# Kernel tuning notes

Hardware: AMD Instinct MI355X
Metric: run time of the kernel (lower is better)

The kernel has to match this reference:

```python
import jax, jax.numpy as jnp
import numpy as np

L, E, K, H, I = 2, 8, 2, 1024, 2048  # stack_size, num_experts, top_k, hidden, intermediate
B, S = 1, 2048


def setup_inputs() -> dict:
    key = jax.random.key(0)
    k0, k1, k2, k3 = jax.random.split(key, 4)
    hidden_states = jax.random.normal(k0, (B, S, H), dtype=jnp.float32)
    router_w = jax.random.normal(k1, (L, H, E), dtype=jnp.float32) * 0.02
    gate_up_proj = jax.random.normal(k2, (L, E, H, 2 * I), dtype=jnp.float32) * (1.0 / np.sqrt(H))
    down_proj = jax.random.normal(k3, (L, E, I, H), dtype=jnp.float32) * (1.0 / np.sqrt(I))
    return {"hidden_states": hidden_states, "router_w": router_w,
            "gate_up_proj": gate_up_proj, "down_proj": down_proj}


def _moe_layer(x, rw, gu_w, dn_w):
    # x: [T,H]; one MoE block: RouterTopK(softmax) + full-capacity top-k GLU expert MLPs
    logits = x @ rw                                   # [T,E] router linear (fp32)
    aff = jax.nn.softmax(logits, axis=-1)
    vals, idx = jax.lax.top_k(aff, K)                 # [T,K]
    vals = vals / jnp.sum(vals, axis=-1, keepdims=True)  # normalize_top_k_affinities=True
    T = x.shape[0]
    # sparse combine weights [T,E]: normalized affinity on chosen experts, 0 elsewhere
    combine = jnp.zeros((T, E), x.dtype).at[jnp.arange(T)[:, None], idx].set(vals)
    gu = jnp.einsum('th,ehi->eti', x, gu_w)           # [E,T,2I] fused gate+up per expert
    gate, up = gu[..., :I], gu[..., I:]
    act = jax.nn.silu(gate) * up                      # GLU with silu
    eo = jnp.einsum('eti,eih->eth', act, dn_w)        # [E,T,H] down proj
    out = jnp.einsum('eth,te->th', eo, combine)       # combine over experts
    return out, logits


def reference(hidden_states, router_w, gate_up_proj, down_proj):
    Bx, Sx, Hx = hidden_states.shape
    x = hidden_states.reshape(-1, Hx)                 # [T,H]
    logits_all = []
    for l in range(L):                                # fixed small stack of layers
        x, logits = _moe_layer(x, router_w[l], gate_up_proj[l], down_proj[l])
        logits_all.append(logits)
    return x.reshape(Bx, Sx, Hx), jnp.stack(logits_all)  # output, [L,T,E] router logits
```

## Files before the change

### kernel.cpp

```cpp
#include <hip/hip_runtime.h>
#include <cstdint>
#include <cstddef>

constexpr int Lc = 2, Ec = 8, Hc = 1024, Ic = 2048, Tc = 2048;

typedef __bf16 bf16x8 __attribute__((ext_vector_type(8)));
typedef float f32x4 __attribute__((ext_vector_type(4)));

__device__ __forceinline__ unsigned short f2bf(float f) {
  unsigned u = __builtin_bit_cast(unsigned, f);
  u = (u + 0x7fffu + ((u >> 16) & 1u)) >> 16;
  return (unsigned short)u;
}
__device__ __forceinline__ float bf2f(unsigned short h) {
  unsigned u = (unsigned)h << 16;
  return __builtin_bit_cast(float, u);
}
__device__ __forceinline__ bf16x8 ldfrag(const unsigned short* p) {
  return __builtin_bit_cast(bf16x8, *(const uint4*)p);
}

__global__ __launch_bounds__(256) void router_kernel(
    const float* __restrict__ x, const float* __restrict__ rw, float* __restrict__ logits,
    unsigned short* __restrict__ xh, unsigned short* __restrict__ xl) {
  const int t = blockIdx.x;
  const int tid = threadIdx.x;
  const float* xr = x + (size_t)t * Hc;
  const int h0 = tid * 4;
  const float4 v = *(const float4*)(xr + h0);
  const float f[4] = {v.x, v.y, v.z, v.w};
  unsigned short hs[4], ls[4];
#pragma unroll
  for (int j = 0; j < 4; ++j) {
    hs[j] = f2bf(f[j]);
    ls[j] = f2bf(f[j] - bf2f(hs[j]));
  }
  *(uint2*)(xh + (size_t)t * Hc + h0) =
      uint2{(unsigned)hs[0] | ((unsigned)hs[1] << 16), (unsigned)hs[2] | ((unsigned)hs[3] << 16)};
  *(uint2*)(xl + (size_t)t * Hc + h0) =
      uint2{(unsigned)ls[0] | ((unsigned)ls[1] << 16), (unsigned)ls[2] | ((unsigned)ls[3] << 16)};

  float acc[Ec];
#pragma unroll
  for (int e = 0; e < Ec; ++e) acc[e] = 0.f;
#pragma unroll
  for (int j = 0; j < 4; ++j) {
    const float* w = rw + (size_t)(h0 + j) * Ec;
#pragma unroll
    for (int e = 0; e < Ec; ++e) acc[e] += f[j] * w[e];
  }
  __shared__ float red[256][Ec];
#pragma unroll
  for (int e = 0; e < Ec; ++e) red[tid][e] = acc[e];
  __syncthreads();
  for (int s = 128; s > 0; s >>= 1) {
    if (tid < s) {
#pragma unroll
      for (int e = 0; e < Ec; ++e) red[tid][e] += red[tid + s][e];
    }
    __syncthreads();
  }
  if (tid < Ec) logits[(size_t)t * Ec + tid] = red[0][tid];
}

__global__ void topk_kernel(const float* __restrict__ logits, int* __restrict__ cnt,
                            int* __restrict__ tokList, float* __restrict__ wList) {
  const int t = blockIdx.x * blockDim.x + threadIdx.x;
  if (t >= Tc) return;
  float l[Ec];
#pragma unroll
  for (int e = 0; e < Ec; ++e) l[e] = logits[(size_t)t * Ec + e];
  float b0 = -3.4e38f, b1 = -3.4e38f;
  int i0 = 0, i1 = 0;
#pragma unroll
  for (int e = 0; e < Ec; ++e) {
    if (l[e] > b0) { b1 = b0; i1 = i0; b0 = l[e]; i0 = e; }
    else if (l[e] > b1) { b1 = l[e]; i1 = e; }
  }
  const float w0 = 1.f / (1.f + expf(b1 - b0));
  const float w1 = 1.f - w0;
  int p0 = atomicAdd(&cnt[i0], 1);
  tokList[i0 * Tc + p0] = t;
  wList[i0 * Tc + p0] = w0;
  int p1 = atomicAdd(&cnt[i1], 1);
  tokList[i1 * Tc + p1] = t;
  wList[i1 * Tc + p1] = w1;
}

__global__ void offsets_kernel(const int* __restrict__ cnt, int* __restrict__ off) {
  if (threadIdx.x == 0) {
    int s = 0;
    for (int e = 0; e < Ec; ++e) { off[e] = s; s += cnt[e]; }
  }
}

template <bool SPLIT>
__global__ __launch_bounds__(256) void wconv_kernel(const float* __restrict__ src,
                                                    unsigned short* __restrict__ dh,
                                                    unsigned short* __restrict__ dl,
                                                    int K, int N) {
  const int e = blockIdx.z;
  const int n0 = blockIdx.x * 64;
  const int k0 = blockIdx.y * 64;
  const int NB = N >> 6, KS = K >> 5;
  src += (size_t)e * K * N;

  __shared__ unsigned short lh[64][66];
  __shared__ unsigned short ll[SPLIT ? 64 : 1][66];
  const int tid = threadIdx.x;

  {
    const int r = tid >> 2, cg = (tid & 3) * 16;
    const float* sp = src + (size_t)(k0 + r) * N + n0 + cg;
#pragma unroll
    for (int i = 0; i < 16; i += 4) {
      const float4 v = *(const float4*)(sp + i);
      const float f[4] = {v.x, v.y, v.z, v.w};
#pragma unroll
      for (int j = 0; j < 4; ++j) {
        const unsigned short h = f2bf(f[j]);
        lh[r][cg + i + j] = h;
        if constexpr (SPLIT) ll[r][cg + i + j] = f2bf(f[j] - bf2f(h));
      }
    }
  }
  __syncthreads();
  {
    const int ksl = tid >> 7, q = (tid >> 5) & 3, n2 = (tid & 31) * 2;
    const int kb = ksl * 32 + q * 8;
    union { unsigned short s[16]; uint4 u[2]; } oh, ol;
#pragma unroll
    for (int s = 0; s < 2; ++s)
#pragma unroll
      for (int i = 0; i < 8; ++i) {
        oh.s[s * 8 + i] = lh[kb + i][n2 + s];
        if constexpr (SPLIT) ol.s[s * 8 + i] = ll[kb + i][n2 + s];
      }
    const size_t cb =
        (((size_t)e * NB + (n0 >> 6)) * KS + (k0 >> 5) + ksl) * 2048 + q * 512 + n2 * 8;
    *(uint4*)(dh + cb) = oh.u[0];
    *(uint4*)(dh + cb + 8) = oh.u[1];
    if constexpr (SPLIT) {
      *(uint4*)(dl + cb) = ol.u[0];
      *(uint4*)(dl + cb + 8) = ol.u[1];
    }
  }
}

template <bool SPLIT>
__global__ __launch_bounds__(256, SPLIT ? 3 : 4) void gateup_kernel(
    const unsigned short* __restrict__ xh, const unsigned short* __restrict__ xl,
    const unsigned short* __restrict__ gwSh, const unsigned short* __restrict__ gwSl,
    const int* __restrict__ cnt, const int* __restrict__ off,
    const int* __restrict__ tokList, unsigned short* __restrict__ actH,
    unsigned short* __restrict__ actL) {
  const int d = blockIdx.x;
  const int lid = (d & 7) * ((int)gridDim.x >> 3) + (d >> 3);
  const int mi = lid & 15;
  const int e = (lid >> 4) & 7;
  const int nb = lid >> 7;
  const int M = cnt[e];
  const int m0 = mi * 128;
  if (m0 >= M) return;
  const int tid = threadIdx.x;
  const int wv = tid >> 6, l64 = tid & 63;
  const int q = l64 >> 4, mr = l64 & 15;
  const int nc = wv * 16 + mr;

  __shared__ __align__(16) unsigned short sAh[2][128 * 40];
  __shared__ __align__(16) unsigned short sAl[2][SPLIT ? 128 * 40 : 8];

  const size_t fragoff = (size_t)(q * 64 + nc) * 8;
  const size_t gBase = (((size_t)e * 64 + nb) * 32) * 2048 + fragoff;
  const size_t uBase = (((size_t)e * 64 + nb + 32) * 32) * 2048 + fragoff;

  const int ar = tid >> 2, ak = (tid & 3) * 8;
  int r0 = m0 + ar;      if (r0 >= M) r0 = M - 1;
  int r1 = m0 + 64 + ar; if (r1 >= M) r1 = M - 1;
  const size_t a0o = (size_t)tokList[e * Tc + r0] * Hc + ak;
  const size_t a1o = (size_t)tokList[e * Tc + r1] * Hc + ak;

  f32x4 accg[8], accu[8];
#pragma unroll
  for (int i = 0; i < 8; ++i) {
    accg[i] = f32x4{0.f, 0.f, 0.f, 0.f};
    accu[i] = f32x4{0.f, 0.f, 0.f, 0.f};
  }

  uint4 paA0h{}, paA1h{}, paA0l{}, paA1l{};
  uint4 paB0h{}, paB1h{}, paB0l{}, paB1l{};
  bf16x8 bcAgh{}, bcAuh{}, bcAgl{}, bcAul{};
  bf16x8 bcBgh{}, bcBuh{}, bcBgl{}, bcBul{};

  paA0h = *(const uint4*)(xh + a0o);
  paA1h = *(const uint4*)(xh + a1o);
  if constexpr (SPLIT) {
    paA0l = *(const uint4*)(xl + a0o);
    paA1l = *(const uint4*)(xl + a1o);
  }
  *(uint4*)&sAh[0][ar * 40 + ak] = paA0h;
  *(uint4*)&sAh[0][(ar + 64) * 40 + ak] = paA1h;
  if constexpr (SPLIT) {
    *(uint4*)&sAl[0][ar * 40 + ak] = paA0l;
    *(uint4*)&sAl[0][(ar + 64) * 40 + ak] = paA1l;
  }
  bcAgh = ldfrag(gwSh + gBase);
  bcAuh = ldfrag(gwSh + uBase);
  if constexpr (SPLIT) {
    bcAgl = ldfrag(gwSl + gBase);
    bcAul = ldfrag(gwSl + uBase);
  }
  paA0h = *(const uint4*)(xh + a0o + 32);
  paA1h = *(const uint4*)(xh + a1o + 32);
  if constexpr (SPLIT) {
    paA0l = *(const uint4*)(xl + a0o + 32);
    paA1l = *(const uint4*)(xl + a1o + 32);
  }
  asm volatile("s_waitcnt lgkmcnt(0)" ::: "memory");
  __builtin_amdgcn_s_barrier();

#define GU_STEP(T, CUR, NX, PA0H, PA1H, PA0L, PA1L, PN0H, PN1H, PN0L, PN1L,             \
                BCGH, BCUH, BCGL, BCUL, BNGH, BNUH, BNGL, BNUL)                         \
  {                                                                                     \
    if ((T) + 1 < 32) {                                                                 \
      BNGH = ldfrag(gwSh + gBase + (size_t)((T) + 1) * 2048);                           \
      BNUH = ldfrag(gwSh + uBase + (size_t)((T) + 1) * 2048);                           \
      if constexpr (SPLIT) {                                                            \
        BNGL = ldfrag(gwSl + gBase + (size_t)((T) + 1) * 2048);                         \
        BNUL = ldfrag(gwSl + uBase + (size_t)((T) + 1) * 2048);                         \
      }                                                                                 \
    }                                                                                   \
    if ((T) + 2 < 32) {                                                                 \
      PN0H = *(const uint4*)(xh + a0o + ((T) + 2) * 32);                                \
      PN1H = *(const uint4*)(xh + a1o + ((T) + 2) * 32);                                \
      if constexpr (SPLIT) {                                                            \
        PN0L = *(const uint4*)(xl + a0o + ((T) + 2) * 32);                              \
        PN1L = *(const uint4*)(xl + a1o + ((T) + 2) * 32);                              \
      }                                                                                 \
    }                                                                                   \
    if ((T) + 1 < 32) {                                                                 \
      *(uint4*)&sAh[NX][ar * 40 + ak] = PA0H;                                           \
      *(uint4*)&sAh[NX][(ar + 64) * 40 + ak] = PA1H;                                    \
      if constexpr (SPLIT) {                                                            \
        *(uint4*)&sAl[NX][ar * 40 + ak] = PA0L;                                         \
        *(uint4*)&sAl[NX][(ar + 64) * 40 + ak] = PA1L;                                  \
      }                                                                                 \
    }                                                                                   \
    __builtin_amdgcn_s_setprio(1);                                                      \
    _Pragma("unroll")                                                                   \
    for (int mt = 0; mt < 8; ++mt) {                                                    \
      const bf16x8 ah = ldfrag(&sAh[CUR][(mt * 16 + mr) * 40 + q * 8]);                 \
      accg[mt] = __builtin_amdgcn_mfma_f32_16x16x32_bf16(ah, BCGH, accg[mt], 0, 0, 0);  \
      accu[mt] = __builtin_amdgcn_mfma_f32_16x16x32_bf16(ah, BCUH, accu[mt], 0, 0, 0);  \
      if constexpr (SPLIT) {                                                            \
        const bf16x8 alr = ldfrag(&sAl[CUR][(mt * 16 + mr) * 40 + q * 8]);              \
        accg[mt] = __builtin_amdgcn_mfma_f32_16x16x32_bf16(ah, BCGL, accg[mt], 0, 0, 0);\
        accg[mt] = __builtin_amdgcn_mfma_f32_16x16x32_bf16(alr, BCGH, accg[mt], 0, 0, 0);\
        accu[mt] = __builtin_amdgcn_mfma_f32_16x16x32_bf16(ah, BCUL, accu[mt], 0, 0, 0);\
        accu[mt] = __builtin_amdgcn_mfma_f32_16x16x32_bf16(alr, BCUH, accu[mt], 0, 0, 0);\
      }                                                                                 \
    }                                                                                   \
    __builtin_amdgcn_s_setprio(0);                                                      \
    if ((T) < 31) {                                                                     \
      asm volatile("s_waitcnt lgkmcnt(0)" ::: "memory");                                \
      __builtin_amdgcn_s_barrier();                                                     \
    }                                                                                   \
  }

  for (int t = 0; t < 32; t += 2) {
    GU_STEP(t, 0, 1, paA0h, paA1h, paA0l, paA1l, paB0h, paB1h, paB0l, paB1l,
            bcAgh, bcAuh, bcAgl, bcAul, bcBgh, bcBuh, bcBgl, bcBul)
    GU_STEP(t + 1, 1, 0, paB0h, paB1h, paB0l, paB1l, paA0h, paA1h, paA0l, paA1l,
            bcBgh, bcBuh, bcBgl, bcBul, bcAgh, bcAuh, bcAgl, bcAul)
  }
#undef GU_STEP

  const int valid = M - m0;
  const int rowbase = off[e] + m0;
#pragma unroll
  for (int mt = 0; mt < 8; ++mt) {
#pragma unroll
    for (int r = 0; r < 4; ++r) {
      const int row = mt * 16 + q * 4 + r;
      if (row < valid) {
        const float g = accg[mt][r];
        const float u = accu[mt][r];
        const float a = (g / (1.f + expf(-g))) * u;
        const size_t idx = (size_t)(rowbase + row) * Ic + (nb * 64 + nc);
        const unsigned short h = f2bf(a);
        actH[idx] = h;
        if constexpr (SPLIT) actL[idx] = f2bf(a - bf2f(h));
      }
    }
  }
}

template <bool SPLIT>
__global__ __launch_bounds__(256, 4) void down_kernel(
    const unsigned short* __restrict__ actH, const unsigned short* __restrict__ actL,
    const unsigned short* __restrict__ dwSh, const unsigned short* __restrict__ dwSl,
    const int* __restrict__ cnt, const int* __restrict__ off,
    const int* __restrict__ tokList, const float* __restrict__ wList,
    float* __restrict__ out) {
  const int d = blockIdx.x;
  const int lid = (d & 7) * ((int)gridDim.x >> 3) + (d >> 3);
  const int mi = lid & 15;
  const int e = (lid >> 4) & 7;
  const int nb = lid >> 7;
  const int M = cnt[e];
  const int m0 = mi * 128;
  if (m0 >= M) return;
  const int tid = threadIdx.x;
  const int wv = tid >> 6, l64 = tid & 63;
  const int q = l64 >> 4, mr = l64 & 15;
  const int nc = wv * 16 + mr;

  __shared__ __align__(16) unsigned short sAh[2][128 * 40];
  __shared__ __align__(16) unsigned short sAl[2][SPLIT ? 128 * 40 : 8];
  __shared__ int sTok[128];
  __shared__ float sW[128];

  if (tid < 128) {
    int r = m0 + tid;
    int rc = r < M ? r : M - 1;
    sTok[tid] = tokList[e * Tc + rc];
    sW[tid] = wList[e * Tc + rc];
  }

  const size_t fragoff = (size_t)(q * 64 + nc) * 8;
  const size_t bBase = (((size_t)e * 16 + nb) * 64) * 2048 + fragoff;
  const int offE = off[e];

  const int ar = tid >> 2, ak = (tid & 3) * 8;
  int r0 = m0 + ar;      if (r0 >= M) r0 = M - 1;
  int r1 = m0 + 64 + ar; if (r1 >= M) r1 = M - 1;
  const size_t a0o = (size_t)(offE + r0) * Ic + ak;
  const size_t a1o = (size_t)(offE + r1) * Ic + ak;

  f32x4 acc[8];
#pragma unroll
  for (int i = 0; i < 8; ++i) acc[i] = f32x4{0.f, 0.f, 0.f, 0.f};

  uint4 paA0h{}, paA1h{}, paA0l{}, paA1l{};
  uint4 paB0h{}, paB1h{}, paB0l{}, paB1l{};
  bf16x8 bcAh{}, bcAl{}, bcBh{}, bcBl{};

  paA0h = *(const uint4*)(actH + a0o);
  paA1h = *(const uint4*)(actH + a1o);
  if constexpr (SPLIT) {
    paA0l = *(const uint4*)(actL + a0o);
    paA1l = *(const uint4*)(actL + a1o);
  }
  *(uint4*)&sAh[0][ar * 40 + ak] = paA0h;
  *(uint4*)&sAh[0][(ar + 64) * 40 + ak] = paA1h;
  if constexpr (SPLIT) {
    *(uint4*)&sAl[0][ar * 40 + ak] = paA0l;
    *(uint4*)&sAl[0][(ar + 64) * 40 + ak] = paA1l;
  }
  bcAh = ldfrag(dwSh + bBase);
  if constexpr (SPLIT) bcAl = ldfrag(dwSl + bBase);
  paA0h = *(const uint4*)(actH + a0o + 32);
  paA1h = *(const uint4*)(actH + a1o + 32);
  if constexpr (SPLIT) {
    paA0l = *(const uint4*)(actL + a0o + 32);
    paA1l = *(const uint4*)(actL + a1o + 32);
  }
  asm volatile("s_waitcnt lgkmcnt(0)" ::: "memory");
  __builtin_amdgcn_s_barrier();

#define DN_STEP(T, CUR, NX, PA0H, PA1H, PA0L, PA1L, PN0H, PN1H, PN0L, PN1L,             \
                BCH, BCL, BNH, BNL)                                                     \
  {                                                                                     \
    if ((T) + 1 < 64) {                                                                 \
      BNH = ldfrag(dwSh + bBase + (size_t)((T) + 1) * 2048);                            \
      if constexpr (SPLIT) BNL = ldfrag(dwSl + bBase + (size_t)((T) + 1) * 2048);       \
    }                                                                                   \
    if ((T) + 2 < 64) {                                                                 \
      PN0H = *(const uint4*)(actH + a0o + ((T) + 2) * 32);                              \
      PN1H = *(const uint4*)(actH + a1o + ((T) + 2) * 32);                              \
      if constexpr (SPLIT) {                                                            \
        PN0L = *(const uint4*)(actL + a0o + ((T) + 2) * 32);                            \
        PN1L = *(const uint4*)(actL + a1o + ((T) + 2) * 32);                            \
      }                                                                                 \
    }                                                                                   \
    if ((T) + 1 < 64) {                                                                 \
      *(uint4*)&sAh[NX][ar * 40 + ak] = PA0H;                                           \
      *(uint4*)&sAh[NX][(ar + 64) * 40 + ak] = PA1H;                                    \
      if constexpr (SPLIT) {                                                            \
        *(uint4*)&sAl[NX][ar * 40 + ak] = PA0L;                                         \
        *(uint4*)&sAl[NX][(ar + 64) * 40 + ak] = PA1L;                                  \
      }                                                                                 \
    }                                                                                   \
    __builtin_amdgcn_s_setprio(1);                                                      \
    _Pragma("unroll")                                                                   \
    for (int mt = 0; mt < 8; ++mt) {                                                    \
      const bf16x8 ah = ldfrag(&sAh[CUR][(mt * 16 + mr) * 40 + q * 8]);                 \
      acc[mt] = __builtin_amdgcn_mfma_f32_16x16x32_bf16(ah, BCH, acc[mt], 0, 0, 0);     \
      if constexpr (SPLIT) {                                                            \
        const bf16x8 alr = ldfrag(&sAl[CUR][(mt * 16 + mr) * 40 + q * 8]);              \
        acc[mt] = __builtin_amdgcn_mfma_f32_16x16x32_bf16(ah, BCL, acc[mt], 0, 0, 0);   \
        acc[mt] = __builtin_amdgcn_mfma_f32_16x16x32_bf16(alr, BCH, acc[mt], 0, 0, 0);  \
      }                                                                                 \
    }                                                                                   \
    __builtin_amdgcn_s_setprio(0);                                                      \
    if ((T) < 63) {                                                                     \
      asm volatile("s_waitcnt lgkmcnt(0)" ::: "memory");                                \
      __builtin_amdgcn_s_barrier();                                                     \
    }                                                                                   \
  }

  for (int t = 0; t < 64; t += 2) {
    DN_STEP(t, 0, 1, paA0h, paA1h, paA0l, paA1l, paB0h, paB1h, paB0l, paB1l,
            bcAh, bcAl, bcBh, bcBl)
    DN_STEP(t + 1, 1, 0, paB0h, paB1h, paB0l, paB1l, paA0h, paA1h, paA0l, paA1l,
            bcBh, bcBl, bcAh, bcAl)
  }
#undef DN_STEP

  const int valid = M - m0;
#pragma unroll
  for (int mt = 0; mt < 8; ++mt) {
#pragma unroll
    for (int r = 0; r < 4; ++r) {
      const int row = mt * 16 + q * 4 + r;
      if (row < valid) {
        atomicAdd(&out[(size_t)sTok[row] * Hc + (nb * 64 + nc)], sW[row] * acc[mt][r]);
      }
    }
  }
}

extern "C" void kernel_launch(void* const* d_in, const int* in_sizes, int n_in, void* d_out,
                              int out_size, void* d_ws, size_t ws_size, hipStream_t stream) {
  const float* x_in = (const float*)d_in[0];
  const float* rw = (const float*)d_in[1];
  const float* guw = (const float*)d_in[2];
  const float* dnw = (const float*)d_in[3];
  float* out = (float*)d_out;
  float* logits_base = out + (size_t)Tc * Hc;

  uint8_t* w = (uint8_t*)d_ws;
  float* x1 = (float*)w;                    w += (size_t)Tc * Hc * 4;
  unsigned short* xh = (unsigned short*)w;  w += (size_t)Tc * Hc * 2;
  unsigned short* xl = (unsigned short*)w;  w += (size_t)Tc * Hc * 2;
  unsigned short* actH = (unsigned short*)w; w += (size_t)Tc * 2 * Ic * 2;
  unsigned short* actL = (unsigned short*)w; w += (size_t)Tc * 2 * Ic * 2;
  int* tokList = (int*)w;                   w += (size_t)Ec * Tc * 4;
  float* wList = (float*)w;                 w += (size_t)Ec * Tc * 4;
  int* cnt0 = (int*)w;                      w += 64;
  int* cnt1 = (int*)w;                      w += 64;
  int* off = (int*)w;                       w += 64;
  unsigned short* wTh = (unsigned short*)w; w += (size_t)Ec * 2 * Ic * Hc * 2;
  unsigned short* wTl = (unsigned short*)w; w += (size_t)Ec * 2 * Ic * Hc * 2;

  hipMemsetAsync(cnt0, 0, 192, stream);
  hipMemsetAsync(x1, 0, (size_t)Tc * Hc * 4, stream);
  hipMemsetAsync(out, 0, (size_t)Tc * Hc * 4, stream);

  router_kernel<<<Tc, 256, 0, stream>>>(x_in, rw, logits_base, xh, xl);
  topk_kernel<<<Tc / 256, 256, 0, stream>>>(logits_base, cnt0, tokList, wList);
  offsets_kernel<<<1, 64, 0, stream>>>(cnt0, off);
  wconv_kernel<true><<<dim3(2 * Ic / 64, Hc / 64, Ec), 256, 0, stream>>>(guw, wTh, wTl, Hc, 2 * Ic);
  gateup_kernel<true><<<16 * 32 * Ec, 256, 0, stream>>>(xh, xl, wTh, wTl, cnt0, off,
                                                        tokList, actH, actL);
  wconv_kernel<true><<<dim3(Hc / 64, Ic / 64, Ec), 256, 0, stream>>>(dnw, wTh, wTl, Ic, Hc);
  down_kernel<true><<<16 * 16 * Ec, 256, 0, stream>>>(actH, actL, wTh, wTl, cnt0,
                                                      off, tokList, wList, x1);

  const float* rw1 = rw + (size_t)Hc * Ec;
  const float* guw1 = guw + (size_t)Ec * Hc * 2 * Ic;
  const float* dnw1 = dnw + (size_t)Ec * Ic * Hc;
  router_kernel<<<Tc, 256, 0, stream>>>(x1, rw1, logits_base + (size_t)Tc * Ec, xh, xl);
  topk_kernel<<<Tc / 256, 256, 0, stream>>>(logits_base + (size_t)Tc * Ec, cnt1, tokList, wList);
  offsets_kernel<<<1, 64, 0, stream>>>(cnt1, off);
  wconv_kernel<false><<<dim3(2 * Ic / 64, Hc / 64, Ec), 256, 0, stream>>>(guw1, wTh, wTl, Hc, 2 * Ic);
  gateup_kernel<false><<<16 * 32 * Ec, 256, 0, stream>>>(xh, xl, wTh, wTl, cnt1, off,
                                                         tokList, actH, actL);
  wconv_kernel<false><<<dim3(Hc / 64, Ic / 64, Ec), 256, 0, stream>>>(dnw1, wTh, wTl, Ic, Hc);
  down_kernel<false><<<16 * 16 * Ec, 256, 0, stream>>>(actH, actL, wTh, wTl, cnt1,
                                                       off, tokList, wList, out);
}
```

Before: 935.2 us.

## Fuse weight conversion blocks into router, gate-up and down kernels

Removes the standalone weight-conversion launches. Each upcoming weight conversion now runs as extra blocks appended to the grid of the preceding compute kernel, so conversion overlaps the router, gate-up or down GEMM and fills idle compute units. Separate A and B weight buffers are used so conversion for the next stage does not overwrite weights still being read. The cost is larger grids, a shared-memory union that may change occupancy, and competition for memory bandwidth with the GEMM blocks.

```diff
diff --git a/kernel.cpp b/kernel.cpp
--- a/kernel.cpp
+++ b/kernel.cpp
@@ -20,10 +20,79 @@
   return __builtin_bit_cast(bf16x8, *(const uint4*)p);
 }
 
+template <bool WSPLIT>
+__device__ __forceinline__ void wconv_block(const float* __restrict__ src,
+                                            unsigned short* __restrict__ dh,
+                                            unsigned short* __restrict__ dl,
+                                            int K, int N, int idx, char* smem) {
+  const int nN = N >> 6, nK = K >> 6;
+  const int sN = 31 - __builtin_clz((unsigned)nN);
+  const int sK = 31 - __builtin_clz((unsigned)nK);
+  const int bx = idx & (nN - 1);
+  const int by = (idx >> sN) & (nK - 1);
+  const int e = idx >> (sN + sK);
+  const int n0 = bx * 64, k0 = by * 64;
+  const int NB = N >> 6, KS = K >> 5;
+  src += (size_t)e * K * N;
+
+  unsigned short(*lh)[66] = (unsigned short(*)[66])smem;
+  unsigned short(*ll)[66] = (unsigned short(*)[66])(smem + 64 * 66 * 2);
+  const int tid = threadIdx.x;
+
+  {
+    const int r = tid >> 2, cg = (tid & 3) * 16;
+    const float* sp = src + (size_t)(k0 + r) * N + n0 + cg;
+#pragma unroll
+    for (int i = 0; i < 16; i += 4) {
+      const float4 v = *(const float4*)(sp + i);
+      const float f[4] = {v.x, v.y, v.z, v.w};
+#pragma unroll
+      for (int j = 0; j < 4; ++j) {
+        const unsigned short h = f2bf(f[j]);
+        lh[r][cg + i + j] = h;
+        if constexpr (WSPLIT) ll[r][cg + i + j] = f2bf(f[j] - bf2f(h));
+      }
+    }
+  }
+  __syncthreads();
+  {
+    const int ksl = tid >> 7, q = (tid >> 5) & 3, n2 = (tid & 31) * 2;
+    const int kb = ksl * 32 + q * 8;
+    union { unsigned short s[16]; uint4 u[2]; } oh, ol;
+#pragma unroll
+    for (int s = 0; s < 2; ++s)
+#pragma unroll
+      for (int i = 0; i < 8; ++i) {
+        oh.s[s * 8 + i] = lh[kb + i][n2 + s];
+        if constexpr (WSPLIT) ol.s[s * 8 + i] = ll[kb + i][n2 + s];
+      }
+    const size_t cb =
+        (((size_t)e * NB + (n0 >> 6)) * KS + (k0 >> 5) + ksl) * 2048 + q * 512 + n2 * 8;
+    *(uint4*)(dh + cb) = oh.u[0];
+    *(uint4*)(dh + cb + 8) = oh.u[1];
+    if constexpr (WSPLIT) {
+      *(uint4*)(dl + cb) = ol.u[0];
+      *(uint4*)(dl + cb + 8) = ol.u[1];
+    }
+  }
+}
+
+template <bool WFUSE>
 __global__ __launch_bounds__(256) void router_kernel(
     const float* __restrict__ x, const float* __restrict__ rw, float* __restrict__ logits,
-    unsigned short* __restrict__ xh, unsigned short* __restrict__ xl) {
-  const int t = blockIdx.x;
+    unsigned short* __restrict__ xh, unsigned short* __restrict__ xl,
+    const float* __restrict__ wsrc, unsigned short* __restrict__ wdh,
+    unsigned short* __restrict__ wdl, int WK, int WN) {
+  __shared__ __align__(16) char smem[WFUSE ? 16896 : 8192];
+  const int bid = blockIdx.x;
+  if constexpr (WFUSE) {
+    if (bid >= Tc) {
+      wconv_block<true>(wsrc, wdh, wdl, WK, WN, bid - Tc, smem);
+      return;
+    }
+  }
+  float(*red)[Ec] = (float(*)[Ec])smem;
+  const int t = bid;
   const int tid = threadIdx.x;
   const float* xr = x + (size_t)t * Hc;
   const int h0 = tid * 4;
@@ -49,7 +118,6 @@
 #pragma unroll
     for (int e = 0; e < Ec; ++e) acc[e] += f[j] * w[e];
   }
-  __shared__ float red[256][Ec];
 #pragma unroll
   for (int e = 0; e < Ec; ++e) red[tid][e] = acc[e];
   __syncthreads();
@@ -94,68 +162,24 @@
   }
 }
 
-template <bool SPLIT>
-__global__ __launch_bounds__(256) void wconv_kernel(const float* __restrict__ src,
-                                                    unsigned short* __restrict__ dh,
-                                                    unsigned short* __restrict__ dl,
-                                                    int K, int N) {
-  const int e = blockIdx.z;
-  const int n0 = blockIdx.x * 64;
-  const int k0 = blockIdx.y * 64;
-  const int NB = N >> 6, KS = K >> 5;
-  src += (size_t)e * K * N;
-
-  __shared__ unsigned short lh[64][66];
-  __shared__ unsigned short ll[SPLIT ? 64 : 1][66];
-  const int tid = threadIdx.x;
-
-  {
-    const int r = tid >> 2, cg = (tid & 3) * 16;
-    const float* sp = src + (size_t)(k0 + r) * N + n0 + cg;
-#pragma unroll
-    for (int i = 0; i < 16; i += 4) {
-      const float4 v = *(const float4*)(sp + i);
-      const float f[4] = {v.x, v.y, v.z, v.w};
-#pragma unroll
-      for (int j = 0; j < 4; ++j) {
-        const unsigned short h = f2bf(f[j]);
-        lh[r][cg + i + j] = h;
-        if constexpr (SPLIT) ll[r][cg + i + j] = f2bf(f[j] - bf2f(h));
-      }
-    }
-  }
-  __syncthreads();
-  {
-    const int ksl = tid >> 7, q = (tid >> 5) & 3, n2 = (tid & 31) * 2;
-    const int kb = ksl * 32 + q * 8;
-    union { unsigned short s[16]; uint4 u[2]; } oh, ol;
-#pragma unroll
-    for (int s = 0; s < 2; ++s)
-#pragma unroll
-      for (int i = 0; i < 8; ++i) {
-        oh.s[s * 8 + i] = lh[kb + i][n2 + s];
-        if constexpr (SPLIT) ol.s[s * 8 + i] = ll[kb + i][n2 + s];
-      }
-    const size_t cb =
-        (((size_t)e * NB + (n0 >> 6)) * KS + (k0 >> 5) + ksl) * 2048 + q * 512 + n2 * 8;
-    *(uint4*)(dh + cb) = oh.u[0];
-    *(uint4*)(dh + cb + 8) = oh.u[1];
-    if constexpr (SPLIT) {
-      *(uint4*)(dl + cb) = ol.u[0];
-      *(uint4*)(dl + cb + 8) = ol.u[1];
-    }
-  }
-}
-
-template <bool SPLIT>
+template <bool SPLIT, bool WFUSE, bool WSPLIT>
 __global__ __launch_bounds__(256, SPLIT ? 3 : 4) void gateup_kernel(
     const unsigned short* __restrict__ xh, const unsigned short* __restrict__ xl,
     const unsigned short* __restrict__ gwSh, const unsigned short* __restrict__ gwSl,
     const int* __restrict__ cnt, const int* __restrict__ off,
     const int* __restrict__ tokList, unsigned short* __restrict__ actH,
-    unsigned short* __restrict__ actL) {
+    unsigned short* __restrict__ actL, const float* __restrict__ wsrc,
+    unsigned short* __restrict__ wdh, unsigned short* __restrict__ wdl, int WK, int WN) {
+  constexpr int GB = 4096;
+  __shared__ __align__(16) char smem[SPLIT ? 40960 : 20480];
   const int d = blockIdx.x;
-  const int lid = (d & 7) * ((int)gridDim.x >> 3) + (d >> 3);
+  if constexpr (WFUSE) {
+    if (d >= GB) {
+      wconv_block<WSPLIT>(wsrc, wdh, wdl, WK, WN, d - GB, smem);
+      return;
+    }
+  }
+  const int lid = (d & 7) * (GB >> 3) + (d >> 3);
   const int mi = lid & 15;
   const int e = (lid >> 4) & 7;
   const int nb = lid >> 7;
@@ -167,8 +191,8 @@
   const int q = l64 >> 4, mr = l64 & 15;
   const int nc = wv * 16 + mr;
 
-  __shared__ __align__(16) unsigned short sAh[2][128 * 40];
-  __shared__ __align__(16) unsigned short sAl[2][SPLIT ? 128 * 40 : 8];
+  unsigned short* sAh = (unsigned short*)smem;
+  unsigned short* sAl = (unsigned short*)(SPLIT ? smem + 20480 : smem);
 
   const size_t fragoff = (size_t)(q * 64 + nc) * 8;
   const size_t gBase = (((size_t)e * 64 + nb) * 32) * 2048 + fragoff;
@@ -198,11 +222,11 @@
     paA0l = *(const uint4*)(xl + a0o);
     paA1l = *(const uint4*)(xl + a1o);
   }
-  *(uint4*)&sAh[0][ar * 40 + ak] = paA0h;
-  *(uint4*)&sAh[0][(ar + 64) * 40 + ak] = paA1h;
-  if constexpr (SPLIT) {
-    *(uint4*)&sAl[0][ar * 40 + ak] = paA0l;
-    *(uint4*)&sAl[0][(ar + 64) * 40 + ak] = paA1l;
+  *(uint4*)&sAh[ar * 40 + ak] = paA0h;
+  *(uint4*)&sAh[(ar + 64) * 40 + ak] = paA1h;
+  if constexpr (SPLIT) {
+    *(uint4*)&sAl[ar * 40 + ak] = paA0l;
+    *(uint4*)&sAl[(ar + 64) * 40 + ak] = paA1l;
   }
   bcAgh = ldfrag(gwSh + gBase);
   bcAuh = ldfrag(gwSh + uBase);
@@ -239,21 +263,21 @@
       }                                                                                 \
     }                                                                                   \
     if ((T) + 1 < 32) {                                                                 \
-      *(uint4*)&sAh[NX][ar * 40 + ak] = PA0H;                                           \
-      *(uint4*)&sAh[NX][(ar + 64) * 40 + ak] = PA1H;                                    \
-      if constexpr (SPLIT) {                                                            \
-        *(uint4*)&sAl[NX][ar * 40 + ak] = PA0L;                                         \
-        *(uint4*)&sAl[NX][(ar + 64) * 40 + ak] = PA1L;                                  \
+      *(uint4*)&sAh[(NX) * 5120 + ar * 40 + ak] = PA0H;                                 \
+      *(uint4*)&sAh[(NX) * 5120 + (ar + 64) * 40 + ak] = PA1H;                          \
+      if constexpr (SPLIT) {                                                            \
+        *(uint4*)&sAl[(NX) * 5120 + ar * 40 + ak] = PA0L;                               \
+        *(uint4*)&sAl[(NX) * 5120 + (ar + 64) * 40 + ak] = PA1L;                        \
       }                                                                                 \
     }                                                                                   \
     __builtin_amdgcn_s_setprio(1);                                                      \
     _Pragma("unroll")                                                                   \
     for (int mt = 0; mt < 8; ++mt) {                                                    \
-      const bf16x8 ah = ldfrag(&sAh[CUR][(mt * 16 + mr) * 40 + q * 8]);                 \
+      const bf16x8 ah = ldfrag(&sAh[(CUR) * 5120 + (mt * 16 + mr) * 40 + q * 8]);       \
       accg[mt] = __builtin_amdgcn_mfma_f32_16x16x32_bf16(ah, BCGH, accg[mt], 0, 0, 0);  \
       accu[mt] = __builtin_amdgcn_mfma_f32_16x16x32_bf16(ah, BCUH, accu[mt], 0, 0, 0);  \
       if constexpr (SPLIT) {                                                            \
-        const bf16x8 alr = ldfrag(&sAl[CUR][(mt * 16 + mr) * 40 + q * 8]);              \
+        const bf16x8 alr = ldfrag(&sAl[(CUR) * 5120 + (mt * 16 + mr) * 40 + q * 8]);    \
         accg[mt] = __builtin_amdgcn_mfma_f32_16x16x32_bf16(ah, BCGL, accg[mt], 0, 0, 0);\
         accg[mt] = __builtin_amdgcn_mfma_f32_16x16x32_bf16(alr, BCGH, accg[mt], 0, 0, 0);\
         accu[mt] = __builtin_amdgcn_mfma_f32_16x16x32_bf16(ah, BCUL, accu[mt], 0, 0, 0);\
@@ -295,15 +319,26 @@
   }
 }
 
-template <bool SPLIT>
+template <bool SPLIT, bool WFUSE, bool WSPLIT>
 __global__ __launch_bounds__(256, 4) void down_kernel(
     const unsigned short* __restrict__ actH, const unsigned short* __restrict__ actL,
     const unsigned short* __restrict__ dwSh, const unsigned short* __restrict__ dwSl,
     const int* __restrict__ cnt, const int* __restrict__ off,
     const int* __restrict__ tokList, const float* __restrict__ wList,
-    float* __restrict__ out) {
+    float* __restrict__ out, const float* __restrict__ wsrc,
+    unsigned short* __restrict__ wdh, unsigned short* __restrict__ wdl, int WK, int WN) {
+  constexpr int GB = 2048;
+  __shared__ __align__(16) char smem[SPLIT ? 40960 : 20480];
+  __shared__ int sTok[128];
+  __shared__ float sW[128];
   const int d = blockIdx.x;
-  const int lid = (d & 7) * ((int)gridDim.x >> 3) + (d >> 3);
+  if constexpr (WFUSE) {
+    if (d >= GB) {
+      wconv_block<WSPLIT>(wsrc, wdh, wdl, WK, WN, d - GB, smem);
+      return;
+    }
+  }
+  const int lid = (d & 7) * (GB >> 3) + (d >> 3);
   const int mi = lid & 15;
   const int e = (lid >> 4) & 7;
   const int nb = lid >> 7;
@@ -315,10 +350,8 @@
   const int q = l64 >> 4, mr = l64 & 15;
   const int nc = wv * 16 + mr;
 
-  __shared__ __align__(16) unsigned short sAh[2][128 * 40];
-  __shared__ __align__(16) unsigned short sAl[2][SPLIT ? 128 * 40 : 8];
-  __shared__ int sTok[128];
-  __shared__ float sW[128];
+  unsigned short* sAh = (unsigned short*)smem;
+  unsigned short* sAl = (unsigned short*)(SPLIT ? smem + 20480 : smem);
 
   if (tid < 128) {
     int r = m0 + tid;
@@ -351,11 +384,11 @@
     paA0l = *(const uint4*)(actL + a0o);
     paA1l = *(const uint4*)(actL + a1o);
   }
-  *(uint4*)&sAh[0][ar * 40 + ak] = paA0h;
-  *(uint4*)&sAh[0][(ar + 64) * 40 + ak] = paA1h;
-  if constexpr (SPLIT) {
-    *(uint4*)&sAl[0][ar * 40 + ak] = paA0l;
-    *(uint4*)&sAl[0][(ar + 64) * 40 + ak] = paA1l;
+  *(uint4*)&sAh[ar * 40 + ak] = paA0h;
+  *(uint4*)&sAh[(ar + 64) * 40 + ak] = paA1h;
+  if constexpr (SPLIT) {
+    *(uint4*)&sAl[ar * 40 + ak] = paA0l;
+    *(uint4*)&sAl[(ar + 64) * 40 + ak] = paA1l;
   }
   bcAh = ldfrag(dwSh + bBase);
   if constexpr (SPLIT) bcAl = ldfrag(dwSl + bBase);
@@ -384,20 +417,20 @@
       }                                                                                 \
     }                                                                                   \
     if ((T) + 1 < 64) {                                                                 \
-      *(uint4*)&sAh[NX][ar * 40 + ak] = PA0H;                                           \
-      *(uint4*)&sAh[NX][(ar + 64) * 40 + ak] = PA1H;                                    \
-      if constexpr (SPLIT) {                                                            \
-        *(uint4*)&sAl[NX][ar * 40 + ak] = PA0L;                                         \
-        *(uint4*)&sAl[NX][(ar + 64) * 40 + ak] = PA1L;                                  \
+      *(uint4*)&sAh[(NX) * 5120 + ar * 40 + ak] = PA0H;                                 \
+      *(uint4*)&sAh[(NX) * 5120 + (ar + 64) * 40 + ak] = PA1H;                          \
+      if constexpr (SPLIT) {                                                            \
+        *(uint4*)&sAl[(NX) * 5120 + ar * 40 + ak] = PA0L;                               \
+        *(uint4*)&sAl[(NX) * 5120 + (ar + 64) * 40 + ak] = PA1L;                        \
       }                                                                                 \
     }                                                                                   \
     __builtin_amdgcn_s_setprio(1);                                                      \
     _Pragma("unroll")                                                                   \
     for (int mt = 0; mt < 8; ++mt) {                                                    \
-      const bf16x8 ah = ldfrag(&sAh[CUR][(mt * 16 + mr) * 40 + q * 8]);                 \
+      const bf16x8 ah = ldfrag(&sAh[(CUR) * 5120 + (mt * 16 + mr) * 40 + q * 8]);       \
       acc[mt] = __builtin_amdgcn_mfma_f32_16x16x32_bf16(ah, BCH, acc[mt], 0, 0, 0);     \
       if constexpr (SPLIT) {                                                            \
-        const bf16x8 alr = ldfrag(&sAl[CUR][(mt * 16 + mr) * 40 + q * 8]);              \
+        const bf16x8 alr = ldfrag(&sAl[(CUR) * 5120 + (mt * 16 + mr) * 40 + q * 8]);    \
         acc[mt] = __builtin_amdgcn_mfma_f32_16x16x32_bf16(ah, BCL, acc[mt], 0, 0, 0);   \
         acc[mt] = __builtin_amdgcn_mfma_f32_16x16x32_bf16(alr, BCH, acc[mt], 0, 0, 0);  \
       }                                                                                 \
@@ -450,33 +483,34 @@
   int* cnt0 = (int*)w;                      w += 64;
   int* cnt1 = (int*)w;                      w += 64;
   int* off = (int*)w;                       w += 64;
-  unsigned short* wTh = (unsigned short*)w; w += (size_t)Ec * 2 * Ic * Hc * 2;
-  unsigned short* wTl = (unsigned short*)w; w += (size_t)Ec * 2 * Ic * Hc * 2;
+  unsigned short* wAh = (unsigned short*)w; w += (size_t)Ec * 2 * Ic * Hc * 2;
+  unsigned short* wAl = (unsigned short*)w; w += (size_t)Ec * 2 * Ic * Hc * 2;
+  unsigned short* wBh = (unsigned short*)w; w += (size_t)Ec * Ic * Hc * 2;
+  unsigned short* wBl = (unsigned short*)w; w += (size_t)Ec * Ic * Hc * 2;
 
   hipMemsetAsync(cnt0, 0, 192, stream);
   hipMemsetAsync(x1, 0, (size_t)Tc * Hc * 4, stream);
   hipMemsetAsync(out, 0, (size_t)Tc * Hc * 4, stream);
 
-  router_kernel<<<Tc, 256, 0, stream>>>(x_in, rw, logits_base, xh, xl);
-  topk_kernel<<<Tc / 256, 256, 0, stream>>>(logits_base, cnt0, tokList, wList);
-  offsets_kernel<<<1, 64, 0, stream>>>(cnt0, off);
-  wconv_kernel<true><<<dim3(2 * Ic / 64, Hc / 64, Ec), 256, 0, stream>>>(guw, wTh, wTl, Hc, 2 * Ic);
-  gateup_kernel<true><<<16 * 32 * Ec, 256, 0, stream>>>(xh, xl, wTh, wTl, cnt0, off,
-                                                        tokList, actH, actL);
-  wconv_kernel<true><<<dim3(Hc / 64, Ic / 64, Ec), 256, 0, stream>>>(dnw, wTh, wTl, Ic, Hc);
-  down_kernel<true><<<16 * 16 * Ec, 256, 0, stream>>>(actH, actL, wTh, wTl, cnt0,
-                                                      off, tokList, wList, x1);
-
   const float* rw1 = rw + (size_t)Hc * Ec;
   const float* guw1 = guw + (size_t)Ec * Hc * 2 * Ic;
   const float* dnw1 = dnw + (size_t)Ec * Ic * Hc;
-  router_kernel<<<Tc, 256, 0, stream>>>(x1, rw1, logits_base + (size_t)Tc * Ec, xh, xl);
+
+  router_kernel<true><<<Tc + 8192, 256, 0, stream>>>(x_in, rw, logits_base, xh, xl,
+                                                     guw, wAh, wAl, Hc, 2 * Ic);
+  topk_kernel<<<Tc / 256, 256, 0, stream>>>(logits_base, cnt0, tokList, wList);
+  offsets_kernel<<<1, 64, 0, stream>>>(cnt0, off);
+  gateup_kernel<true, true, true><<<4096 + 4096, 256, 0, stream>>>(
+      xh, xl, wAh, wAl, cnt0, off, tokList, actH, actL, dnw, wBh, wBl, Ic, Hc);
+  down_kernel<true, true, false><<<2048 + 8192, 256, 0, stream>>>(
+      actH, actL, wBh, wBl, cnt0, off, tokList, wList, x1, guw1, wAh, nullptr, Hc, 2 * Ic);
+
+  router_kernel<false><<<Tc, 256, 0, stream>>>(x1, rw1, logits_base + (size_t)Tc * Ec, xh, xl,
+                                               nullptr, nullptr, nullptr, 0, 0);
   topk_kernel<<<Tc / 256, 256, 0, stream>>>(logits_base + (size_t)Tc * Ec, cnt1, tokList, wList);
   offsets_kernel<<<1, 64, 0, stream>>>(cnt1, off);
-  wconv_kernel<false><<<dim3(2 * Ic / 64, Hc / 64, Ec), 256, 0, stream>>>(guw1, wTh, wTl, Hc, 2 * Ic);
-  gateup_kernel<false><<<16 * 32 * Ec, 256, 0, stream>>>(xh, xl, wTh, wTl, cnt1, off,
-                                                         tokList, actH, actL);
-  wconv_kernel<false><<<dim3(Hc / 64, Ic / 64, Ec), 256, 0, stream>>>(dnw1, wTh, wTl, Ic, Hc);
-  down_kernel<false><<<16 * 16 * Ec, 256, 0, stream>>>(actH, actL, wTh, wTl, cnt1,
-                                                       off, tokList, wList, out);
-}
+  gateup_kernel<false, true, false><<<4096 + 4096, 256, 0, stream>>>(
+      xh, xl, wAh, wAl, cnt1, off, tokList, actH, actL, dnw1, wBh, nullptr, Ic, Hc);
+  down_kernel<false, false, false><<<2048, 256, 0, stream>>>(
+      actH, actL, wBh, wBl, cnt1, off, tokList, wList, out, nullptr, nullptr, nullptr, 0, 0);
+}
```

New measurement: 888.0 us (median of 3 runs). 5.0% less time.
